# Kernel optimization log

Measured on AMD Instinct MI355X. Metric: run time of the kernel, lower is better.

The kernel has to match this reference:

```python
import jax, jax.numpy as jnp
import numpy as np

B = 8192          # batch
CIN = 256         # in_channels
COUT = 64         # out_channels
K = 3             # kernel_size
NK = 4            # num_kernels
HIDDEN = int(CIN * 0.25)   # attention hidden = int(in_channels*ratio) = 64
TEMP = 34.0       # attention temperature
KAN_IN = 64 * 4   # base*4 = flattened conv output (COUT*2*2)
GRID_SIZE, SPLINE_ORDER = 5, 3
GMIN, GMAX = -1.0, 1.0
NUM_BASES = GRID_SIZE + SPLINE_ORDER  # 8


def setup_inputs() -> dict:
    key = jax.random.key(0)
    ks = jax.random.split(key, 8)
    s = 0.05
    return {
        "x": jax.random.normal(ks[0], (B, CIN, 4, 4), jnp.float32),
        # dynamic-conv kernel bank [num_kernels, out, in, k, k]
        "weight": jax.random.normal(ks[1], (NK, COUT, CIN, K, K), jnp.float32) * s,
        "bias": jnp.zeros((NK, COUT), jnp.float32),
        # Attention2D: GAP -> fc1 (1x1 conv == linear) -> ReLU -> fc2 -> softmax(/T)
        "fc1_w": jax.random.normal(ks[2], (HIDDEN, CIN), jnp.float32) * s,
        "fc1_b": jnp.zeros((HIDDEN,), jnp.float32),
        "fc2_w": jax.random.normal(ks[3], (NK, HIDDEN), jnp.float32) * s,
        "fc2_b": jnp.zeros((NK,), jnp.float32),
        # KANLinear params (efficient-KAN style)
        "kan_base_w": jax.random.normal(ks[4], (COUT, KAN_IN), jnp.float32) * s,
        "kan_spline_w": jax.random.normal(ks[5], (COUT, KAN_IN, NUM_BASES), jnp.float32) * s,
        "kan_spline_scaler": jnp.ones((COUT, KAN_IN), jnp.float32),
    }


def _bspline_bases(x):
    """Cox-de Boor B-spline bases; x [B, F] -> [B, F, GRID_SIZE+SPLINE_ORDER]."""
    h = (GMAX - GMIN) / GRID_SIZE
    # extended grid, shared across features: length grid_size + 2*order + 1 = 12
    grid = jnp.arange(-SPLINE_ORDER, GRID_SIZE + SPLINE_ORDER + 1, dtype=x.dtype) * h + GMIN
    xe = x[..., None]  # [B, F, 1]
    bases = ((xe >= grid[:-1]) & (xe < grid[1:])).astype(x.dtype)  # order 0
    for k in range(1, SPLINE_ORDER + 1):
        left = (xe - grid[: -(k + 1)]) / (grid[k:-1] - grid[: -(k + 1)]) * bases[..., :-1]
        right = (grid[k + 1:] - xe) / (grid[k + 1:] - grid[1:-k]) * bases[..., 1:]
        bases = left + right
    return bases  # [B, F, 8]


def reference(x, weight, bias, fc1_w, fc1_b, fc2_w, fc2_b,
              kan_base_w, kan_spline_w, kan_spline_scaler):
    b = x.shape[0]
    # --- Attention2D: softmax over kernel bank ---
    pooled = x.mean(axis=(2, 3))                                  # [B, CIN]
    hid = jax.nn.relu(pooled @ fc1_w.T + fc1_b)                   # [B, HIDDEN]
    attn = jax.nn.softmax((hid @ fc2_w.T + fc2_b) / TEMP, axis=-1)  # [B, NK]
    # --- per-sample dynamic conv, fused form ---
    # sum_k a[b,k] * conv(x, W_k) == conv with per-sample aggregated weight
    w_all = weight.reshape(NK * COUT, CIN, K, K)
    y = jax.lax.conv_general_dilated(
        x, w_all, window_strides=(1, 1), padding="VALID",
        dimension_numbers=("NCHW", "OIHW", "NCHW"))                # [B, NK*COUT, 2, 2]
    y = y.reshape(b, NK, COUT, y.shape[-2], y.shape[-1])
    conv_out = jnp.einsum("bk,bkohw->bohw", attn, y)
    conv_out = conv_out + (attn @ bias)[:, :, None, None]          # aggregated bias
    # --- KANLinear on flattened conv output ---
    feat = conv_out.reshape(b, -1)                                 # [B, 256]
    base_out = jax.nn.silu(feat) @ kan_base_w.T                    # [B, COUT]
    bases = _bspline_bases(feat)                                   # [B, 256, 8]
    spline_out = jnp.einsum("big,oig->bo", bases,
                            kan_spline_w * kan_spline_scaler[..., None])
    return base_out + spline_out                                   # [B, COUT]
```

## Files before the change

### kernel.cpp

```cpp
#include <hip/hip_runtime.h>

#define BT   8192
#define MS   16
#define XBUF (MS * 656)

typedef _Float16 half8  __attribute__((ext_vector_type(8)));
typedef _Float16 half4v __attribute__((ext_vector_type(4)));
typedef float    floatx2  __attribute__((ext_vector_type(2)));
typedef float    floatx4  __attribute__((ext_vector_type(4)));
typedef float    floatx16 __attribute__((ext_vector_type(16)));

__device__ __forceinline__ int slotOff(int f) {
    return 256 + ((f ^ ((f >> 3) & 7)) << 3);
}

__global__ __launch_bounds__(256) void prep_kernel(
    const float* __restrict__ weight, const float* __restrict__ base_w,
    const float* __restrict__ spline_w, const float* __restrict__ scaler,
    const float* __restrict__ fc1_w,
    _Float16* __restrict__ W3, _Float16* __restrict__ Wk3,
    _Float16* __restrict__ Wf3)
{
    const int bb = blockIdx.x;
    const int tid = threadIdx.x;
    if (bb < 256) {
        const int n = bb;
        const int c = tid;
        const float* src = weight + ((size_t)n * 256 + c) * 9;
        const int cc = c >> 5, ci = c & 31;
        #pragma unroll
        for (int ij = 0; ij < 9; ++ij) {
            W3[((size_t)(cc * 9 + ij) * 256 + n) * 32 + ci] = (_Float16)src[ij];
        }
    } else if (bb < 328) {
        const int st = bb - 256;
        #pragma unroll
        for (int u = 0; u < 8; ++u) {
            const int idx = u * 256 + tid;
            const int n = idx >> 5, kk = idx & 31;
            const int k = st * 32 + kk;
            float v;
            if (k < 256) {
                v = base_w[n * 256 + k];
            } else {
                const int r = k - 256;
                const int i = r >> 3, g = r & 7;
                v = spline_w[((size_t)n * 256 + i) * 8 + g] * scaler[n * 256 + i];
            }
            Wk3[(size_t)st * 2048 + idx] = (_Float16)v;
        }
    } else {
        const int st2 = bb - 328;
        #pragma unroll
        for (int u = 0; u < 8; ++u) {
            const int idx = u * 256 + tid;
            const int n = idx >> 5, kk = idx & 31;
            Wf3[(size_t)st2 * 2048 + idx] = (_Float16)fc1_w[n * 256 + st2 * 32 + kk];
        }
    }
}

__device__ __forceinline__ void bases8c(float xv, _Float16* dst) {
    const float t = (xv + 2.2f) * 2.5f;
    const float ft = floorf(t);
    const int idx = (int)ft;
    const float u = t - ft, v = 1.f - u;
    const float u2 = u * u, v2 = v * v;
    const float c3 = u2 * u * (1.f / 6.f);
    const float c2 = (1.f / 6.f) + 0.5f * (u + u2 - u2 * u);
    const float c1 = (1.f / 6.f) + 0.5f * (v + v2 - v2 * v);
    const float c0 = v2 * v * (1.f / 6.f);
    half8 hb;
    #pragma unroll
    for (int tt = 0; tt < 8; ++tt) {
        const int d = idx - tt;
        float b = 0.f;
        b = (d == 0) ? c3 : b;
        b = (d == 1) ? c2 : b;
        b = (d == 2) ? c1 : b;
        b = (d == 3) ? c0 : b;
        hb[tt] = (_Float16)b;
    }
    *(half8*)dst = hb;
}

__global__ __launch_bounds__(512, 4) void fused_kernel(
    const float* __restrict__ x, const _Float16* __restrict__ W3,
    const _Float16* __restrict__ Wk3, const _Float16* __restrict__ Wf3,
    const float* __restrict__ bias, const float* __restrict__ fc1_b,
    const float* __restrict__ fc2_w, const float* __restrict__ fc2_b,
    float* __restrict__ out)
{
    __shared__ __align__(16) char smem[MS * 2312 * 2];
    __shared__ float hid_lds[MS * 68];
    __shared__ float attn_s[MS][4];

    _Float16* Xs  = (_Float16*)smem;
    _Float16* Pl  = (_Float16*)(smem + 2 * XBUF * 2);
    _Float16* Act = (_Float16*)smem;

    const int tid = threadIdx.x;
    const int wv = tid >> 6, lane = tid & 63;
    const int nl = lane & 15, q = lane >> 4;
    const int cg = wv & 3, rh = wv >> 2;
    const int b0i = blockIdx.x * MS;

    const int posr = nl & 3;
    const int aLane = (nl >> 2) * 656 + ((posr >> 1) * 4 + (posr & 1)) * 40 + q * 8;
    const int lbW0 = (((rh * 2 + 0) * 4 + cg) * 16 + nl) * 32 + q * 8;
    const int lbW1 = (((rh * 2 + 1) * 4 + cg) * 16 + nl) * 32 + q * 8;

    const int s_ = tid >> 5, cch = tid & 31;
    const float* xg = x + ((size_t)(b0i + s_) * 256 + cch) * 16;

    floatx4 acc[4][2];
    #pragma unroll
    for (int rt = 0; rt < 4; ++rt) {
        acc[rt][0] = floatx4{0.f, 0.f, 0.f, 0.f};
        acc[rt][1] = floatx4{0.f, 0.f, 0.f, 0.f};
    }

    half8 bA0 = *(const half8*)(W3 + lbW0);
    half8 bB0 = *(const half8*)(W3 + lbW1);
    half8 bA1 = *(const half8*)(W3 + 8192 + lbW0);
    half8 bB1 = *(const half8*)(W3 + 8192 + lbW1);

    floatx16 r = *(const floatx16*)xg;
    {
        _Float16* xd = &Xs[s_ * 656 + cch];
        #pragma unroll
        for (int p = 0; p < 16; ++p) xd[p * 40] = (_Float16)r[p];
        float sm = 0.f;
        #pragma unroll
        for (int p = 0; p < 16; ++p) sm += r[p];
        Pl[s_ * 264 + cch] = (_Float16)(sm * (1.0f / 16.0f));
    }
    r = *(const floatx16*)(xg + 512);
    __syncthreads();

    #pragma unroll 1
    for (int cc = 0; cc < 8; ++cc) {
        const int cur = cc & 1;
        if (cc < 7) {
            _Float16* xd = &Xs[(cur ^ 1) * XBUF + s_ * 656 + cch];
            #pragma unroll
            for (int p = 0; p < 16; ++p) xd[p * 40] = (_Float16)r[p];
            float sm = 0.f;
            #pragma unroll
            for (int p = 0; p < 16; ++p) sm += r[p];
            Pl[s_ * 264 + (cc + 1) * 32 + cch] = (_Float16)(sm * (1.0f / 16.0f));
        }
        if (cc < 6) r = *(const floatx16*)(xg + (cc + 2) * 512);

        const _Float16* wst = W3 + (size_t)cc * 9 * 8192;
        const _Float16* xb = &Xs[cur * XBUF + aLane];

        const int p0tab[9] = {0, 1, 2, 4, 5, 6, 8, 9, 10};

        #pragma unroll
        for (int ij = 0; ij < 9; ++ij) {
            const _Float16* wnx = (cc * 9 + ij + 2 < 72)
                                ? (wst + (size_t)(ij + 2) * 8192)
                                : W3;
            half8 bA2 = *(const half8*)(wnx + lbW0);
            half8 bB2 = *(const half8*)(wnx + lbW1);

            const int p0 = p0tab[ij];
            half8 aF[4];
            #pragma unroll
            for (int rt = 0; rt < 4; ++rt)
                aF[rt] = *(const half8*)&xb[rt * 2624 + p0 * 40];
            #pragma unroll
            for (int rt = 0; rt < 4; ++rt) {
                acc[rt][0] = __builtin_amdgcn_mfma_f32_16x16x32_f16(aF[rt], bA0, acc[rt][0], 0, 0, 0);
                acc[rt][1] = __builtin_amdgcn_mfma_f32_16x16x32_f16(aF[rt], bB0, acc[rt][1], 0, 0, 0);
            }
            bA0 = bA1; bB0 = bB1; bA1 = bA2; bB1 = bB2;
        }
        __syncthreads();
    }

    if (rh == 0) {
        floatx4 a1 = floatx4{0.f, 0.f, 0.f, 0.f};
        const _Float16* wfb = Wf3 + ((cg * 16 + nl) * 32 + q * 8);
        const _Float16* pb = &Pl[nl * 264 + q * 8];
        #pragma unroll
        for (int st = 0; st < 8; ++st) {
            const half8 aF = *(const half8*)(pb + st * 32);
            const half8 bF = *(const half8*)(wfb + st * 2048);
            a1 = __builtin_amdgcn_mfma_f32_16x16x32_f16(aF, bF, a1, 0, 0, 0);
        }
        const int h = cg * 16 + nl;
        const float fb = fc1_b[h];
        #pragma unroll
        for (int reg = 0; reg < 4; ++reg)
            hid_lds[(q * 4 + reg) * 68 + h] = fmaxf(a1[reg] + fb, 0.f);
    }
    __syncthreads();

    if (wv == 0) {
        const int s = lane >> 2, kb = lane & 3;
        float l = fc2_b[kb];
        #pragma unroll 8
        for (int h = 0; h < 64; ++h) l += hid_lds[s * 68 + h] * fc2_w[kb * 64 + h];
        float m = fmaxf(l, __shfl_xor(l, 1));
        m = fmaxf(m, __shfl_xor(m, 2));
        const float e = __expf((l - m) * (1.0f / 34.0f));
        float sm = e + __shfl_xor(e, 1);
        sm += __shfl_xor(sm, 2);
        attn_s[s][kb] = e / sm;
    }
    const int o = cg * 16 + nl;
    #pragma unroll
    for (int rt = 0; rt < 4; ++rt) {
        const int s = rt * 4 + q;
        #pragma unroll
        for (int e = 0; e < 4; ++e) {
            floatx2 pr; pr[0] = acc[rt][0][e]; pr[1] = acc[rt][1][e];
            float* fp = (float*)&Act[s * 2312 + slotOff(o * 4 + e)];
            *(floatx2*)(fp + rh * 2) = pr;
        }
    }
    __syncthreads();

    {
        const int sl = lane >> 5, fl = lane & 31;
        const int s = wv * 2 + sl;
        const float a0 = attn_s[s][0], a1 = attn_s[s][1],
                    a2 = attn_s[s][2], a3 = attn_s[s][3];
        const int o0 = fl * 2, f0 = fl * 8;
        const float badd0 = a0 * bias[o0] + a1 * bias[64 + o0]
                          + a2 * bias[128 + o0] + a3 * bias[192 + o0];
        const float badd1 = a0 * bias[o0 + 1] + a1 * bias[64 + o0 + 1]
                          + a2 * bias[128 + o0 + 1] + a3 * bias[192 + o0 + 1];
        half8 sv;
        #pragma unroll
        for (int u = 0; u < 8; ++u) {
            float* fp = (float*)&Act[s * 2312 + slotOff(f0 + u)];
            const floatx4 P = *(const floatx4*)fp;
            const float fv = a0 * P[0] + a1 * P[1] + a2 * P[2] + a3 * P[3]
                           + ((u < 4) ? badd0 : badd1);
            const float ex = __expf(-fv);
            sv[u] = (_Float16)(fv * __builtin_amdgcn_rcpf(1.f + ex));
            bases8c(fv, (_Float16*)fp);
        }
        *(half8*)&Act[s * 2312 + o0 * 4] = sv;
    }
    __syncthreads();

    {
        floatx4 a2 = floatx4{0.f, 0.f, 0.f, 0.f};
        const _Float16* wkb = Wk3 + ((size_t)(cg * 16 + nl) * 32 + q * 8);
        const _Float16* abr = &Act[nl * 2312];
        const int st0 = rh * 36;
        half8 kb0 = *(const half8*)(wkb + (size_t)st0 * 2048);
        half8 kb1 = *(const half8*)(wkb + (size_t)(st0 + 1) * 2048);
        #pragma unroll 4
        for (int i = 0; i < 36; ++i) {
            const int st = st0 + i;
            half8 kb2;
            if (i < 34) kb2 = *(const half8*)(wkb + (size_t)(st + 2) * 2048);
            const _Float16* ap;
            if (st < 8) {
                ap = abr + st * 32 + q * 8;
            } else {
                const int f  = st * 4 + q - 32;
                const int fx = f ^ (((st - 8) >> 1) & 7);
                ap = abr + 256 + (fx << 3);
            }
            const half8 aF = *(const half8*)ap;
            a2 = __builtin_amdgcn_mfma_f32_16x16x32_f16(aF, kb0, a2, 0, 0, 0);
            kb0 = kb1; kb1 = kb2;
        }
        if (rh == 1) *(floatx4*)&hid_lds[cg * 256 + lane * 4] = a2;
        __syncthreads();
        if (rh == 0) {
            const floatx4 p = *(const floatx4*)&hid_lds[cg * 256 + lane * 4];
            a2 = a2 + p;
            #pragma unroll
            for (int reg = 0; reg < 4; ++reg)
                out[(size_t)(b0i + q * 4 + reg) * 64 + cg * 16 + nl] = a2[reg];
        }
    }
}

extern "C" void kernel_launch(void* const* d_in, const int* in_sizes, int n_in,
                              void* d_out, int out_size, void* d_ws, size_t ws_size,
                              hipStream_t stream) {
    const float* x          = (const float*)d_in[0];
    const float* weight     = (const float*)d_in[1];
    const float* bias       = (const float*)d_in[2];
    const float* fc1_w      = (const float*)d_in[3];
    const float* fc1_b      = (const float*)d_in[4];
    const float* fc2_w      = (const float*)d_in[5];
    const float* fc2_b      = (const float*)d_in[6];
    const float* kan_base_w = (const float*)d_in[7];
    const float* kan_spline = (const float*)d_in[8];
    const float* kan_scaler = (const float*)d_in[9];
    float* out = (float*)d_out;

    _Float16* W3  = (_Float16*)d_ws;
    _Float16* Wk3 = W3 + (size_t)72 * 8192;
    _Float16* Wf3 = Wk3 + (size_t)72 * 2048;

    prep_kernel<<<336, 256, 0, stream>>>(weight, kan_base_w, kan_spline,
                                         kan_scaler, fc1_w, W3, Wk3, Wf3);
    fused_kernel<<<BT / MS, 512, 0, stream>>>(x, W3, Wk3, Wf3, bias, fc1_b,
                                              fc2_w, fc2_b, out);
}
```

Before: 245.6 us.

## Shrink LDS footprint by processing KAN epilogue in two halves for occupancy

The KAN epilogue now handles the 16-sample tile as two passes of 8 samples. This lets the activation/bases buffer be reused and shrinks shared memory to about 50 KB. The hidden fc1 activations are stored as fp16, and the exchange and attention buffers are packed into the same shared array. Launch bounds are raised from 4 to 6 blocks per CU to get more occupancy. The cost is extra barriers and MFMA passes in which half the rows are redundant, since nl&7 duplicates rows and only q<2 lanes write out. There is also more register pressure under the tighter bound.

```diff
diff --git a/kernel.cpp b/kernel.cpp
--- a/kernel.cpp
+++ b/kernel.cpp
@@ -84,20 +84,21 @@
     *(half8*)dst = hb;
 }
 
-__global__ __launch_bounds__(512, 4) void fused_kernel(
+__global__ __launch_bounds__(512, 6) void fused_kernel(
     const float* __restrict__ x, const _Float16* __restrict__ W3,
     const _Float16* __restrict__ Wk3, const _Float16* __restrict__ Wf3,
     const float* __restrict__ bias, const float* __restrict__ fc1_b,
     const float* __restrict__ fc2_w, const float* __restrict__ fc2_b,
     float* __restrict__ out)
 {
-    __shared__ __align__(16) char smem[MS * 2312 * 2];
-    __shared__ float hid_lds[MS * 68];
-    __shared__ float attn_s[MS][4];
-
-    _Float16* Xs  = (_Float16*)smem;
-    _Float16* Pl  = (_Float16*)(smem + 2 * XBUF * 2);
-    _Float16* Act = (_Float16*)smem;
+    __shared__ __align__(16) char smem[50688];
+
+    _Float16* Xs    = (_Float16*)smem;
+    _Float16* Pl    = (_Float16*)(smem + 41984);
+    _Float16* Act   = (_Float16*)smem;
+    _Float16* hid16 = (_Float16*)(smem + 36992);
+    float (*attn_s)[4] = (float(*)[4])(smem + 39168);
+    float* exch     = (float*)(smem + 41984);
 
     const int tid = threadIdx.x;
     const int wv = tid >> 6, lane = tid & 63;
@@ -194,93 +195,99 @@
         const float fb = fc1_b[h];
         #pragma unroll
         for (int reg = 0; reg < 4; ++reg)
-            hid_lds[(q * 4 + reg) * 68 + h] = fmaxf(a1[reg] + fb, 0.f);
+            hid16[(q * 4 + reg) * 68 + h] = (_Float16)fmaxf(a1[reg] + fb, 0.f);
     }
     __syncthreads();
 
-    if (wv == 0) {
-        const int s = lane >> 2, kb = lane & 3;
-        float l = fc2_b[kb];
-        #pragma unroll 8
-        for (int h = 0; h < 64; ++h) l += hid_lds[s * 68 + h] * fc2_w[kb * 64 + h];
-        float m = fmaxf(l, __shfl_xor(l, 1));
-        m = fmaxf(m, __shfl_xor(m, 2));
-        const float e = __expf((l - m) * (1.0f / 34.0f));
-        float sm = e + __shfl_xor(e, 1);
-        sm += __shfl_xor(sm, 2);
-        attn_s[s][kb] = e / sm;
-    }
     const int o = cg * 16 + nl;
+
     #pragma unroll
-    for (int rt = 0; rt < 4; ++rt) {
-        const int s = rt * 4 + q;
-        #pragma unroll
-        for (int e = 0; e < 4; ++e) {
-            floatx2 pr; pr[0] = acc[rt][0][e]; pr[1] = acc[rt][1][e];
-            float* fp = (float*)&Act[s * 2312 + slotOff(o * 4 + e)];
-            *(floatx2*)(fp + rh * 2) = pr;
-        }
-    }
-    __syncthreads();
-
-    {
-        const int sl = lane >> 5, fl = lane & 31;
-        const int s = wv * 2 + sl;
-        const float a0 = attn_s[s][0], a1 = attn_s[s][1],
-                    a2 = attn_s[s][2], a3 = attn_s[s][3];
-        const int o0 = fl * 2, f0 = fl * 8;
-        const float badd0 = a0 * bias[o0] + a1 * bias[64 + o0]
-                          + a2 * bias[128 + o0] + a3 * bias[192 + o0];
-        const float badd1 = a0 * bias[o0 + 1] + a1 * bias[64 + o0 + 1]
-                          + a2 * bias[128 + o0 + 1] + a3 * bias[192 + o0 + 1];
-        half8 sv;
-        #pragma unroll
-        for (int u = 0; u < 8; ++u) {
-            float* fp = (float*)&Act[s * 2312 + slotOff(f0 + u)];
-            const floatx4 P = *(const floatx4*)fp;
-            const float fv = a0 * P[0] + a1 * P[1] + a2 * P[2] + a3 * P[3]
-                           + ((u < 4) ? badd0 : badd1);
-            const float ex = __expf(-fv);
-            sv[u] = (_Float16)(fv * __builtin_amdgcn_rcpf(1.f + ex));
-            bases8c(fv, (_Float16*)fp);
-        }
-        *(half8*)&Act[s * 2312 + o0 * 4] = sv;
-    }
-    __syncthreads();
-
-    {
-        floatx4 a2 = floatx4{0.f, 0.f, 0.f, 0.f};
-        const _Float16* wkb = Wk3 + ((size_t)(cg * 16 + nl) * 32 + q * 8);
-        const _Float16* abr = &Act[nl * 2312];
-        const int st0 = rh * 36;
-        half8 kb0 = *(const half8*)(wkb + (size_t)st0 * 2048);
-        half8 kb1 = *(const half8*)(wkb + (size_t)(st0 + 1) * 2048);
-        #pragma unroll 4
-        for (int i = 0; i < 36; ++i) {
-            const int st = st0 + i;
-            half8 kb2;
-            if (i < 34) kb2 = *(const half8*)(wkb + (size_t)(st + 2) * 2048);
-            const _Float16* ap;
-            if (st < 8) {
-                ap = abr + st * 32 + q * 8;
-            } else {
-                const int f  = st * 4 + q - 32;
-                const int fx = f ^ (((st - 8) >> 1) & 7);
-                ap = abr + 256 + (fx << 3);
-            }
-            const half8 aF = *(const half8*)ap;
-            a2 = __builtin_amdgcn_mfma_f32_16x16x32_f16(aF, kb0, a2, 0, 0, 0);
-            kb0 = kb1; kb1 = kb2;
-        }
-        if (rh == 1) *(floatx4*)&hid_lds[cg * 256 + lane * 4] = a2;
+    for (int hh = 0; hh < 2; ++hh) {
+        if (hh == 0 && wv == 0) {
+            const int s = lane >> 2, kb = lane & 3;
+            float l = fc2_b[kb];
+            #pragma unroll 8
+            for (int h = 0; h < 64; ++h)
+                l += (float)hid16[s * 68 + h] * fc2_w[kb * 64 + h];
+            float m = fmaxf(l, __shfl_xor(l, 1));
+            m = fmaxf(m, __shfl_xor(m, 2));
+            const float e = __expf((l - m) * (1.0f / 34.0f));
+            float sm = e + __shfl_xor(e, 1);
+            sm += __shfl_xor(sm, 2);
+            attn_s[s][kb] = e / sm;
+        }
+        #pragma unroll
+        for (int r2 = 0; r2 < 2; ++r2) {
+            const int sl = r2 * 4 + q;
+            #pragma unroll
+            for (int e = 0; e < 4; ++e) {
+                floatx2 pr;
+                pr[0] = acc[hh * 2 + r2][0][e];
+                pr[1] = acc[hh * 2 + r2][1][e];
+                float* fp = (float*)&Act[sl * 2312 + slotOff(o * 4 + e)];
+                *(floatx2*)(fp + rh * 2) = pr;
+            }
+        }
         __syncthreads();
-        if (rh == 0) {
-            const floatx4 p = *(const floatx4*)&hid_lds[cg * 256 + lane * 4];
-            a2 = a2 + p;
-            #pragma unroll
-            for (int reg = 0; reg < 4; ++reg)
-                out[(size_t)(b0i + q * 4 + reg) * 64 + cg * 16 + nl] = a2[reg];
-        }
+
+        {
+            const int sg = hh * 8 + wv;
+            const float a0 = attn_s[sg][0], a1 = attn_s[sg][1],
+                        a2 = attn_s[sg][2], a3 = attn_s[sg][3];
+            const int f0 = lane * 4;
+            const float badd = a0 * bias[lane] + a1 * bias[64 + lane]
+                             + a2 * bias[128 + lane] + a3 * bias[192 + lane];
+            half4v sv;
+            #pragma unroll
+            for (int u = 0; u < 4; ++u) {
+                float* fp = (float*)&Act[wv * 2312 + slotOff(f0 + u)];
+                const floatx4 P = *(const floatx4*)fp;
+                const float fv = a0 * P[0] + a1 * P[1] + a2 * P[2] + a3 * P[3]
+                               + badd;
+                const float ex = __expf(-fv);
+                sv[u] = (_Float16)(fv * __builtin_amdgcn_rcpf(1.f + ex));
+                bases8c(fv, (_Float16*)fp);
+            }
+            *(half4v*)&Act[wv * 2312 + lane * 4] = sv;
+        }
+        __syncthreads();
+
+        {
+            floatx4 a2 = floatx4{0.f, 0.f, 0.f, 0.f};
+            const _Float16* wkb = Wk3 + ((size_t)(cg * 16 + nl) * 32 + q * 8);
+            const _Float16* abr = &Act[(nl & 7) * 2312];
+            const int st0 = rh * 36;
+            half8 kb0 = *(const half8*)(wkb + (size_t)st0 * 2048);
+            half8 kb1 = *(const half8*)(wkb + (size_t)(st0 + 1) * 2048);
+            #pragma unroll 4
+            for (int i = 0; i < 36; ++i) {
+                const int st = st0 + i;
+                half8 kb2;
+                if (i < 34) kb2 = *(const half8*)(wkb + (size_t)(st + 2) * 2048);
+                const _Float16* ap;
+                if (st < 8) {
+                    ap = abr + st * 32 + q * 8;
+                } else {
+                    const int f  = st * 4 + q - 32;
+                    const int fx = f ^ (((st - 8) >> 1) & 7);
+                    ap = abr + 256 + (fx << 3);
+                }
+                const half8 aF = *(const half8*)ap;
+                a2 = __builtin_amdgcn_mfma_f32_16x16x32_f16(aF, kb0, a2, 0, 0, 0);
+                kb0 = kb1; kb1 = kb2;
+            }
+            if (rh == 1) *(floatx4*)&exch[cg * 256 + lane * 4] = a2;
+            __syncthreads();
+            if (rh == 0 && q < 2) {
+                const floatx4 p = *(const floatx4*)&exch[cg * 256 + lane * 4];
+                a2 = a2 + p;
+                #pragma unroll
+                for (int reg = 0; reg < 4; ++reg)
+                    out[(size_t)(b0i + hh * 8 + q * 4 + reg) * 64 + cg * 16 + nl]
+                        = a2[reg];
+            }
+        }
+        if (hh == 0) __syncthreads();
     }
 }
 
```

Measured after the change: 283.3 us. 1.15x slower.

## Double block to 1024 threads, splitting sample rows across wave pairs

Applied to the files above, without the earlier changes.

Raises the fused kernel to 1024 threads per block. The extra waves each own half of the sample row tiles in the conv MFMA loop, so each wave holds 2x2 accumulators instead of 4x2. The x staging is spread over more lanes using 8-float loads plus a shuffle reduction, and the weight prefetch depth drops from two steps to one. The aim is to cut per-wave register pressure and add latency hiding, at the cost of loading each B-weight fragment twice and leaving half the waves idle in the KAN GEMM tail.

```diff
diff --git a/kernel.cpp b/kernel.cpp
--- a/kernel.cpp
+++ b/kernel.cpp
@@ -8,7 +8,7 @@
 typedef _Float16 half4v __attribute__((ext_vector_type(4)));
 typedef float    floatx2  __attribute__((ext_vector_type(2)));
 typedef float    floatx4  __attribute__((ext_vector_type(4)));
-typedef float    floatx16 __attribute__((ext_vector_type(16)));
+typedef float    floatx8  __attribute__((ext_vector_type(8)));
 
 __device__ __forceinline__ int slotOff(int f) {
     return 256 + ((f ^ ((f >> 3) & 7)) << 3);
@@ -84,7 +84,7 @@
     *(half8*)dst = hb;
 }
 
-__global__ __launch_bounds__(512, 4) void fused_kernel(
+__global__ __launch_bounds__(1024, 8) void fused_kernel(
     const float* __restrict__ x, const _Float16* __restrict__ W3,
     const _Float16* __restrict__ Wk3, const _Float16* __restrict__ Wf3,
     const float* __restrict__ bias, const float* __restrict__ fc1_b,
@@ -102,55 +102,57 @@
     const int tid = threadIdx.x;
     const int wv = tid >> 6, lane = tid & 63;
     const int nl = lane & 15, q = lane >> 4;
-    const int cg = wv & 3, rh = wv >> 2;
+    const int cg = wv & 3, rh = (wv >> 2) & 1, rp = wv >> 3;
     const int b0i = blockIdx.x * MS;
 
     const int posr = nl & 3;
-    const int aLane = (nl >> 2) * 656 + ((posr >> 1) * 4 + (posr & 1)) * 40 + q * 8;
+    const int aLane = (nl >> 2) * 656 + ((posr >> 1) * 4 + (posr & 1)) * 40
+                    + q * 8 + rp * 5248;
     const int lbW0 = (((rh * 2 + 0) * 4 + cg) * 16 + nl) * 32 + q * 8;
     const int lbW1 = (((rh * 2 + 1) * 4 + cg) * 16 + nl) * 32 + q * 8;
 
-    const int s_ = tid >> 5, cch = tid & 31;
-    const float* xg = x + ((size_t)(b0i + s_) * 256 + cch) * 16;
-
-    floatx4 acc[4][2];
+    const int s_ = wv, cch = lane >> 1, ph = lane & 1;
+    const float* xg = x + ((size_t)(b0i + s_) * 256 + cch) * 16 + ph * 8;
+
+    floatx4 acc[2][2];
     #pragma unroll
-    for (int rt = 0; rt < 4; ++rt) {
-        acc[rt][0] = floatx4{0.f, 0.f, 0.f, 0.f};
-        acc[rt][1] = floatx4{0.f, 0.f, 0.f, 0.f};
+    for (int r2 = 0; r2 < 2; ++r2) {
+        acc[r2][0] = floatx4{0.f, 0.f, 0.f, 0.f};
+        acc[r2][1] = floatx4{0.f, 0.f, 0.f, 0.f};
     }
 
     half8 bA0 = *(const half8*)(W3 + lbW0);
     half8 bB0 = *(const half8*)(W3 + lbW1);
-    half8 bA1 = *(const half8*)(W3 + 8192 + lbW0);
-    half8 bB1 = *(const half8*)(W3 + 8192 + lbW1);
-
-    floatx16 r = *(const floatx16*)xg;
+
+    floatx8 r = *(const floatx8*)xg;
     {
-        _Float16* xd = &Xs[s_ * 656 + cch];
-        #pragma unroll
-        for (int p = 0; p < 16; ++p) xd[p * 40] = (_Float16)r[p];
+        _Float16* xd = &Xs[s_ * 656 + ph * 320 + cch];
+        #pragma unroll
+        for (int p = 0; p < 8; ++p) xd[p * 40] = (_Float16)r[p];
         float sm = 0.f;
         #pragma unroll
-        for (int p = 0; p < 16; ++p) sm += r[p];
-        Pl[s_ * 264 + cch] = (_Float16)(sm * (1.0f / 16.0f));
-    }
-    r = *(const floatx16*)(xg + 512);
+        for (int p = 0; p < 8; ++p) sm += r[p];
+        sm += __shfl_xor(sm, 1);
+        if (ph == 0) Pl[s_ * 264 + cch] = (_Float16)(sm * (1.0f / 16.0f));
+    }
+    r = *(const floatx8*)(xg + 512);
     __syncthreads();
 
     #pragma unroll 1
     for (int cc = 0; cc < 8; ++cc) {
         const int cur = cc & 1;
         if (cc < 7) {
-            _Float16* xd = &Xs[(cur ^ 1) * XBUF + s_ * 656 + cch];
+            _Float16* xd = &Xs[(cur ^ 1) * XBUF + s_ * 656 + ph * 320 + cch];
             #pragma unroll
-            for (int p = 0; p < 16; ++p) xd[p * 40] = (_Float16)r[p];
+            for (int p = 0; p < 8; ++p) xd[p * 40] = (_Float16)r[p];
             float sm = 0.f;
             #pragma unroll
-            for (int p = 0; p < 16; ++p) sm += r[p];
-            Pl[s_ * 264 + (cc + 1) * 32 + cch] = (_Float16)(sm * (1.0f / 16.0f));
-        }
-        if (cc < 6) r = *(const floatx16*)(xg + (cc + 2) * 512);
+            for (int p = 0; p < 8; ++p) sm += r[p];
+            sm += __shfl_xor(sm, 1);
+            if (ph == 0)
+                Pl[s_ * 264 + (cc + 1) * 32 + cch] = (_Float16)(sm * (1.0f / 16.0f));
+        }
+        if (cc < 6) r = *(const floatx8*)(xg + (cc + 2) * 512);
 
         const _Float16* wst = W3 + (size_t)cc * 9 * 8192;
         const _Float16* xb = &Xs[cur * XBUF + aLane];
@@ -159,28 +161,25 @@
 
         #pragma unroll
         for (int ij = 0; ij < 9; ++ij) {
-            const _Float16* wnx = (cc * 9 + ij + 2 < 72)
-                                ? (wst + (size_t)(ij + 2) * 8192)
+            const _Float16* wnx = (cc * 9 + ij + 1 < 72)
+                                ? (wst + (size_t)(ij + 1) * 8192)
                                 : W3;
-            half8 bA2 = *(const half8*)(wnx + lbW0);
-            half8 bB2 = *(const half8*)(wnx + lbW1);
+            half8 nA = *(const half8*)(wnx + lbW0);
+            half8 nB = *(const half8*)(wnx + lbW1);
 
             const int p0 = p0tab[ij];
-            half8 aF[4];
-            #pragma unroll
-            for (int rt = 0; rt < 4; ++rt)
-                aF[rt] = *(const half8*)&xb[rt * 2624 + p0 * 40];
-            #pragma unroll
-            for (int rt = 0; rt < 4; ++rt) {
-                acc[rt][0] = __builtin_amdgcn_mfma_f32_16x16x32_f16(aF[rt], bA0, acc[rt][0], 0, 0, 0);
-                acc[rt][1] = __builtin_amdgcn_mfma_f32_16x16x32_f16(aF[rt], bB0, acc[rt][1], 0, 0, 0);
-            }
-            bA0 = bA1; bB0 = bB1; bA1 = bA2; bB1 = bB2;
+            const half8 aF0 = *(const half8*)&xb[p0 * 40];
+            const half8 aF1 = *(const half8*)&xb[2624 + p0 * 40];
+            acc[0][0] = __builtin_amdgcn_mfma_f32_16x16x32_f16(aF0, bA0, acc[0][0], 0, 0, 0);
+            acc[0][1] = __builtin_amdgcn_mfma_f32_16x16x32_f16(aF0, bB0, acc[0][1], 0, 0, 0);
+            acc[1][0] = __builtin_amdgcn_mfma_f32_16x16x32_f16(aF1, bA0, acc[1][0], 0, 0, 0);
+            acc[1][1] = __builtin_amdgcn_mfma_f32_16x16x32_f16(aF1, bB0, acc[1][1], 0, 0, 0);
+            bA0 = nA; bB0 = nB;
         }
         __syncthreads();
     }
 
-    if (rh == 0) {
+    if (rh == 0 && rp == 0) {
         floatx4 a1 = floatx4{0.f, 0.f, 0.f, 0.f};
         const _Float16* wfb = Wf3 + ((cg * 16 + nl) * 32 + q * 8);
         const _Float16* pb = &Pl[nl * 264 + q * 8];
@@ -212,11 +211,11 @@
     }
     const int o = cg * 16 + nl;
     #pragma unroll
-    for (int rt = 0; rt < 4; ++rt) {
-        const int s = rt * 4 + q;
+    for (int r2 = 0; r2 < 2; ++r2) {
+        const int s = (rp * 2 + r2) * 4 + q;
         #pragma unroll
         for (int e = 0; e < 4; ++e) {
-            floatx2 pr; pr[0] = acc[rt][0][e]; pr[1] = acc[rt][1][e];
+            floatx2 pr; pr[0] = acc[r2][0][e]; pr[1] = acc[r2][1][e];
             float* fp = (float*)&Act[s * 2312 + slotOff(o * 4 + e)];
             *(floatx2*)(fp + rh * 2) = pr;
         }
@@ -224,32 +223,28 @@
     __syncthreads();
 
     {
-        const int sl = lane >> 5, fl = lane & 31;
-        const int s = wv * 2 + sl;
-        const float a0 = attn_s[s][0], a1 = attn_s[s][1],
-                    a2 = attn_s[s][2], a3 = attn_s[s][3];
-        const int o0 = fl * 2, f0 = fl * 8;
-        const float badd0 = a0 * bias[o0] + a1 * bias[64 + o0]
-                          + a2 * bias[128 + o0] + a3 * bias[192 + o0];
-        const float badd1 = a0 * bias[o0 + 1] + a1 * bias[64 + o0 + 1]
-                          + a2 * bias[128 + o0 + 1] + a3 * bias[192 + o0 + 1];
-        half8 sv;
-        #pragma unroll
-        for (int u = 0; u < 8; ++u) {
-            float* fp = (float*)&Act[s * 2312 + slotOff(f0 + u)];
+        const float a0 = attn_s[wv][0], a1 = attn_s[wv][1],
+                    a2 = attn_s[wv][2], a3 = attn_s[wv][3];
+        const int f0 = lane * 4;
+        const float badd = a0 * bias[lane] + a1 * bias[64 + lane]
+                         + a2 * bias[128 + lane] + a3 * bias[192 + lane];
+        half4v sv;
+        #pragma unroll
+        for (int u = 0; u < 4; ++u) {
+            float* fp = (float*)&Act[wv * 2312 + slotOff(f0 + u)];
             const floatx4 P = *(const floatx4*)fp;
             const float fv = a0 * P[0] + a1 * P[1] + a2 * P[2] + a3 * P[3]
-                           + ((u < 4) ? badd0 : badd1);
+                           + badd;
             const float ex = __expf(-fv);
             sv[u] = (_Float16)(fv * __builtin_amdgcn_rcpf(1.f + ex));
             bases8c(fv, (_Float16*)fp);
         }
-        *(half8*)&Act[s * 2312 + o0 * 4] = sv;
-    }
-    __syncthreads();
-
-    {
-        floatx4 a2 = floatx4{0.f, 0.f, 0.f, 0.f};
+        *(half4v*)&Act[wv * 2312 + lane * 4] = sv;
+    }
+    __syncthreads();
+
+    floatx4 a2 = floatx4{0.f, 0.f, 0.f, 0.f};
+    if (rp == 0) {
         const _Float16* wkb = Wk3 + ((size_t)(cg * 16 + nl) * 32 + q * 8);
         const _Float16* abr = &Act[nl * 2312];
         const int st0 = rh * 36;
@@ -273,14 +268,14 @@
             kb0 = kb1; kb1 = kb2;
         }
         if (rh == 1) *(floatx4*)&hid_lds[cg * 256 + lane * 4] = a2;
-        __syncthreads();
-        if (rh == 0) {
-            const floatx4 p = *(const floatx4*)&hid_lds[cg * 256 + lane * 4];
-            a2 = a2 + p;
-            #pragma unroll
-            for (int reg = 0; reg < 4; ++reg)
-                out[(size_t)(b0i + q * 4 + reg) * 64 + cg * 16 + nl] = a2[reg];
-        }
+    }
+    __syncthreads();
+    if (rp == 0 && rh == 0) {
+        const floatx4 p = *(const floatx4*)&hid_lds[cg * 256 + lane * 4];
+        a2 = a2 + p;
+        #pragma unroll
+        for (int reg = 0; reg < 4; ++reg)
+            out[(size_t)(b0i + q * 4 + reg) * 64 + cg * 16 + nl] = a2[reg];
     }
 }
 
@@ -305,6 +300,6 @@
 
     prep_kernel<<<336, 256, 0, stream>>>(weight, kan_base_w, kan_spline,
                                          kan_scaler, fc1_w, W3, Wk3, Wf3);
-    fused_kernel<<<BT / MS, 512, 0, stream>>>(x, W3, Wk3, Wf3, bias, fc1_b,
-                                              fc2_w, fc2_b, out);
-}
+    fused_kernel<<<BT / MS, 1024, 0, stream>>>(x, W3, Wk3, Wf3, bias, fc1_b,
+                                               fc2_w, fc2_b, out);
+}
```

Measured after the change: 281.9 us. 14.8% more time.
